# Performance work log

Measured on AMD Instinct MI355X. Metric: run time of the kernel, lower is better.

The kernel has to match this reference:

```python
import jax, jax.numpy as jnp
import numpy as np


def _bipolarize(x):
    # torchhd.hard_quantize: sign quantize to {-1, +1}
    return jnp.where(x > 0, 1.0, -1.0).astype(x.dtype)


def _transform(am, projections):
    """PQ-HDC Algorithm 1: MAP AM (C,D) -> binary AM (C,P,D) in {0,1} + weights (C,P)."""
    C, D = am.shape

    def per_class(hv):  # hv: (D,)
        bips = []
        loss = hv
        for _ in range(projections):  # P is small (2-4), sequential by construction
            bip = _bipolarize(loss)
            dot = jnp.dot(loss, bip)
            # orthogonal projection of loss onto bip: bip * dot / ||bip||^2
            loss = loss - bip * dot / jnp.sum(bip * bip)
            bips.append(bip)
        X = jnp.stack(bips)  # (P, D) bipolar
        G = X @ X.T  # (P, P)
        w = hv @ X.T @ jnp.linalg.inv(G)  # (P,)
        # normalize: length of w[:,None]*X over full (P,D) matrix
        length = jnp.linalg.norm(w[:, None] * X)
        w = jnp.sqrt(jnp.asarray(D, hv.dtype)) * w / length
        w = w ** 2
        return X, w

    Xs, ws = jax.vmap(per_class)(am)  # (C,P,D), (C,P)
    ambin = jnp.where(Xs > 0, 1.0, 0.0).astype(am.dtype)  # binarize {0,1}
    return ambin, ws


def _phs(qbin, ambin, weights):
    """Pseudo Hamming Similarity, batched. qbin:(B,D) {0,1}; ambin:(C,P,D) {0,1}."""
    D = qbin.shape[-1]
    # equal-bit count = D - sum(q XOR a) = D - sum_q - sum_a + 2*q.a
    dots = jnp.einsum('bd,cpd->bcp', qbin, ambin)  # (B,C,P)
    qsum = jnp.sum(qbin, axis=-1)                  # (B,)
    asum = jnp.sum(ambin, axis=-1)                 # (C,P)
    ham = D - qsum[:, None, None] - asum[None, :, :] + 2.0 * dots
    return jnp.sum(weights[None, :, :] * ham, axis=-1)  # (B,C)


def setup_inputs() -> dict:
    key = jax.random.key(0)
    k1, k2 = jax.random.split(key)
    B, C, D = 4096, 128, 10000
    query = jax.random.normal(k1, (B, D), dtype=jnp.float32)
    am = jax.random.normal(k2, (C, D), dtype=jnp.float32)
    return {"query": query, "am": am, "projections": 3}


def reference(query, am, projections):
    ambin, weights = _transform(am, projections)
    qbin = jnp.where(_bipolarize(query) > 0, 1.0, 0.0).astype(query.dtype)
    return _phs(qbin, ambin, weights)  # (B, C) logits
```

## Files before the change

kernel.cpp:

```cpp
#include <hip/hip_runtime.h>
#include <stdint.h>

typedef unsigned long long u64;

#define D_DIM   10000
#define C_CLS   128
#define WPRP    192
#define NWORDS  160
#define NIT     40

__device__ __forceinline__ float wred64(float v) {
#pragma unroll
    for (int m = 1; m <= 32; m <<= 1) v += __shfl_xor(v, m);
    return v;
}
__device__ __forceinline__ int wred64i(int v) {
#pragma unroll
    for (int m = 1; m <= 32; m <<= 1) v += __shfl_xor(v, m);
    return v;
}

__device__ __forceinline__ size_t am_idx(int c, int wi, int p) {
    return ((size_t)c * 32 + (unsigned)wi / 6u) * 18 + (size_t)p * 6 + (unsigned)wi % 6u;
}

__global__ __launch_bounds__(256) void kA_transform(const float* __restrict__ am,
                                                    u64* __restrict__ amw,
                                                    float4* __restrict__ wtab)
{
    const int c = blockIdx.x;
    const int t = threadIdx.x;
    const int w = t >> 6;
    const int l = t & 63;

    __shared__ float redf[4];
    __shared__ int   sI[4][6];
    __shared__ float sF[4][3];

    const float* hvp = am + (size_t)c * D_DIM;

    float4 loss[10], hv[10];
#pragma unroll
    for (int k = 0; k < 10; ++k) {
        const int it = w + 4 * k;
        const int d0 = it * 256 + 4 * l;
        float4 x = make_float4(0.f, 0.f, 0.f, 0.f);
        if (d0 + 3 < D_DIM) x = *(const float4*)(hvp + d0);
        loss[k] = x; hv[k] = x;
    }

    int cnt[3]; float hX[3]; u64 sp[3];

#pragma unroll
    for (int p = 0; p < 3; ++p) {
        float sabs = 0.f;
#pragma unroll
        for (int k = 0; k < 10; ++k)
            sabs += fabsf(loss[k].x) + fabsf(loss[k].y) + fabsf(loss[k].z) + fabsf(loss[k].w);
        sabs = wred64(sabs);
        if (l == 0) redf[w] = sabs;
        __syncthreads();
        const float dot = redf[0] + redf[1] + redf[2] + redf[3];
        __syncthreads();
        const float dd = dot / (float)D_DIM;

        u64 bits = 0; int cc = 0; float hx = 0.f;
#pragma unroll
        for (int k = 0; k < 10; ++k) {
            const int it = w + 4 * k;
            const bool p0 = loss[k].x > 0.f;
            const bool p1 = loss[k].y > 0.f;
            const bool p2 = loss[k].z > 0.f;
            const bool p3 = loss[k].w > 0.f;
            const u64 b0 = __ballot(p0);
            const u64 b1 = __ballot(p1);
            const u64 b2 = __ballot(p2);
            const u64 b3 = __ballot(p3);
            if (l < 4) {
                const u64 bb = (l == 0) ? b0 : ((l == 1) ? b1 : ((l == 2) ? b2 : b3));
                amw[am_idx(c, it * 4 + l, p)] = bb;
            }
            bits |= ((u64)p0 << (4 * k)) | ((u64)p1 << (4 * k + 1))
                  | ((u64)p2 << (4 * k + 2)) | ((u64)p3 << (4 * k + 3));
            cc += (int)p0 + (int)p1 + (int)p2 + (int)p3;
            hx += (p0 ? hv[k].x : -hv[k].x) + (p1 ? hv[k].y : -hv[k].y)
                + (p2 ? hv[k].z : -hv[k].z) + (p3 ? hv[k].w : -hv[k].w);
            float4 L = loss[k];
            L.x -= p0 ? dd : -dd; L.y -= p1 ? dd : -dd;
            L.z -= p2 ? dd : -dd; L.w -= p3 ? dd : -dd;
            const int d0 = it * 256 + 4 * l;
            if (!(d0 + 3 < D_DIM)) L = make_float4(0.f, 0.f, 0.f, 0.f);
            loss[k] = L;
        }
        if (t < WPRP - NWORDS) amw[am_idx(c, NWORDS + t, p)] = 0ull;
        sp[p] = bits; cnt[p] = cc; hX[p] = hx;
    }

    int vi[6] = { cnt[0], cnt[1], cnt[2],
                  static_cast<int>(__popcll(sp[0] ^ sp[1])),
                  static_cast<int>(__popcll(sp[0] ^ sp[2])),
                  static_cast<int>(__popcll(sp[1] ^ sp[2])) };
#pragma unroll
    for (int i = 0; i < 6; ++i) vi[i] = wred64i(vi[i]);
    float vf[3] = { hX[0], hX[1], hX[2] };
#pragma unroll
    for (int i = 0; i < 3; ++i) vf[i] = wred64(vf[i]);
    if (l == 0) {
#pragma unroll
        for (int i = 0; i < 6; ++i) sI[w][i] = vi[i];
#pragma unroll
        for (int i = 0; i < 3; ++i) sF[w][i] = vf[i];
    }
    __syncthreads();
    if (t == 0) {
        int a0 = 0, a1 = 0, a2 = 0, X01 = 0, X02 = 0, X12 = 0;
        float h0f = 0, h1f = 0, h2f = 0;
        for (int i = 0; i < 4; ++i) {
            a0 += sI[i][0]; a1 += sI[i][1]; a2 += sI[i][2];
            X01 += sI[i][3]; X02 += sI[i][4]; X12 += sI[i][5];
            h0f += sF[i][0]; h1f += sF[i][1]; h2f += sF[i][2];
        }
        const double Dv = (double)D_DIM;
        const double h0 = h0f, h1 = h1f, h2 = h2f;
        const double g01 = Dv - 2.0 * X01, g02 = Dv - 2.0 * X02, g12 = Dv - 2.0 * X12;
        const double A00 = Dv * Dv - g12 * g12;
        const double A01 = g02 * g12 - g01 * Dv;
        const double A02 = g01 * g12 - g02 * Dv;
        const double A11 = Dv * Dv - g02 * g02;
        const double A12 = g02 * g01 - Dv * g12;
        const double A22 = Dv * Dv - g01 * g01;
        const double det = Dv * A00 + g01 * A01 + g02 * A02;
        const double w0 = (A00 * h0 + A01 * h1 + A02 * h2) / det;
        const double w1 = (A01 * h0 + A11 * h1 + A12 * h2) / det;
        const double w2 = (A02 * h0 + A12 * h1 + A22 * h2) / det;
        const double s = w0 * w0 + w1 * w1 + w2 * w2;
        const double f0 = w0 * w0 / s, f1 = w1 * w1 / s, f2 = w2 * w2 / s;
        const double cb = -(f0 * a0 + f1 * a1 + f2 * a2);
        wtab[c] = make_float4((float)f0, (float)f1, (float)f2, (float)cb);
    }
}

__global__ __launch_bounds__(256, 4) void kB_phs(const float* __restrict__ query,
                                                 const u64* __restrict__ amw,
                                                 const float4* __restrict__ wtab,
                                                 float* __restrict__ out)
{
    __shared__ u64 qlds[4 * WPRP];
    __shared__ float4 wsh[C_CLS];
    const int t = threadIdx.x;
    const int w = t >> 6;
    const int l = t & 63;
    const int r0 = blockIdx.x * 4;

    if (t < C_CLS) wsh[t] = wtab[t];

    {
        const float* qp = query + (size_t)(r0 + w) * D_DIM;
        u64* qrow = qlds + w * WPRP;
        for (int it = 0; it < NIT; ++it) {
            const int d0 = it * 256 + 4 * l;
            float4 x = make_float4(0.f, 0.f, 0.f, 0.f);
            if (d0 + 3 < D_DIM) x = *(const float4*)(qp + d0);
            const u64 b0 = __ballot(x.x > 0.f);
            const u64 b1 = __ballot(x.y > 0.f);
            const u64 b2 = __ballot(x.z > 0.f);
            const u64 b3 = __ballot(x.w > 0.f);
            if (l < 4) qrow[it * 4 + l] = (l == 0) ? b0 : ((l == 1) ? b1 : ((l == 2) ? b2 : b3));
        }
        if (l < 32) qrow[NWORDS + l] = 0ull;
    }
    __syncthreads();

    const int wl = l & 31;
    const int rh = l >> 5;
    const int rA = 2 * rh, rB = 2 * rh + 1;

    const u64* qa = qlds + rA * WPRP + wl * 6;
    const u64* qb = qlds + rB * WPRP + wl * 6;
    const u64 qa0 = qa[0], qa1 = qa[1], qa2 = qa[2], qa3 = qa[3], qa4 = qa[4], qa5 = qa[5];
    const u64 qb0 = qb[0], qb1 = qb[1], qb2 = qb[2], qb3 = qb[3], qb4 = qb[4], qb5 = qb[5];

    float sA = (float)(__popcll(qa0) + __popcll(qa1) + __popcll(qa2) +
                       __popcll(qa3) + __popcll(qa4) + __popcll(qa5));
    float sB = (float)(__popcll(qb0) + __popcll(qb1) + __popcll(qb2) +
                       __popcll(qb3) + __popcll(qb4) + __popcll(qb5));
#pragma unroll
    for (int m = 1; m <= 16; m <<= 1) { sA += __shfl_xor(sA, m); sB += __shfl_xor(sB, m); }
    const float baseA = (float)D_DIM - sA;
    const float baseB = (float)D_DIM - sB;

    float* orowA = out + (size_t)(r0 + rA) * C_CLS;
    float* orowB = out + (size_t)(r0 + rB) * C_CLS;

    const int c0 = 32 * w;
#pragma unroll 2
    for (int i = 0; i < 32; ++i) {
        const int c = c0 + i;
        const u64* ap = amw + ((size_t)c * 32 + wl) * 18;
        const ulonglong2 v0 = *(const ulonglong2*)(ap + 0);
        const ulonglong2 v1 = *(const ulonglong2*)(ap + 2);
        const ulonglong2 v2 = *(const ulonglong2*)(ap + 4);
        const ulonglong2 v3 = *(const ulonglong2*)(ap + 6);
        const ulonglong2 v4 = *(const ulonglong2*)(ap + 8);
        const ulonglong2 v5 = *(const ulonglong2*)(ap + 10);
        const ulonglong2 v6 = *(const ulonglong2*)(ap + 12);
        const ulonglong2 v7 = *(const ulonglong2*)(ap + 14);
        const ulonglong2 v8 = *(const ulonglong2*)(ap + 16);

        const int pA0 = (int)(__popcll(qa0 & v0.x) + __popcll(qa1 & v0.y) + __popcll(qa2 & v1.x)
                      + __popcll(qa3 & v1.y) + __popcll(qa4 & v2.x) + __popcll(qa5 & v2.y));
        const int pA1 = (int)(__popcll(qa0 & v3.x) + __popcll(qa1 & v3.y) + __popcll(qa2 & v4.x)
                      + __popcll(qa3 & v4.y) + __popcll(qa4 & v5.x) + __popcll(qa5 & v5.y));
        const int pA2 = (int)(__popcll(qa0 & v6.x) + __popcll(qa1 & v6.y) + __popcll(qa2 & v7.x)
                      + __popcll(qa3 & v7.y) + __popcll(qa4 & v8.x) + __popcll(qa5 & v8.y));
        const int pB0 = (int)(__popcll(qb0 & v0.x) + __popcll(qb1 & v0.y) + __popcll(qb2 & v1.x)
                      + __popcll(qb3 & v1.y) + __popcll(qb4 & v2.x) + __popcll(qb5 & v2.y));
        const int pB1 = (int)(__popcll(qb0 & v3.x) + __popcll(qb1 & v3.y) + __popcll(qb2 & v4.x)
                      + __popcll(qb3 & v4.y) + __popcll(qb4 & v5.x) + __popcll(qb5 & v5.y));
        const int pB2 = (int)(__popcll(qb0 & v6.x) + __popcll(qb1 & v6.y) + __popcll(qb2 & v7.x)
                      + __popcll(qb3 & v7.y) + __popcll(qb4 & v8.x) + __popcll(qb5 & v8.y));

        const float4 wv = wsh[c];
        float partA = wv.x * (float)pA0 + wv.y * (float)pA1 + wv.z * (float)pA2;
        float partB = wv.x * (float)pB0 + wv.y * (float)pB1 + wv.z * (float)pB2;
#pragma unroll
        for (int m = 1; m <= 16; m <<= 1) {
            partA += __shfl_xor(partA, m);
            partB += __shfl_xor(partB, m);
        }
        if (wl == 0) {
            orowA[c] = baseA + wv.w + 2.f * partA;
            orowB[c] = baseB + wv.w + 2.f * partB;
        }
    }
}

extern "C" void kernel_launch(void* const* d_in, const int* in_sizes, int n_in,
                              void* d_out, int out_size, void* d_ws, size_t ws_size,
                              hipStream_t stream)
{
    const float* query = (const float*)d_in[0];
    const float* am    = (const float*)d_in[1];
    float* out = (float*)d_out;

    float4* wtab = (float4*)d_ws;
    u64* amw = (u64*)((char*)d_ws + 2048);

    const int B = in_sizes[0] / D_DIM;

    hipLaunchKernelGGL(kA_transform, dim3(C_CLS), dim3(256), 0, stream, am, amw, wtab);
    hipLaunchKernelGGL(kB_phs, dim3(B / 4), dim3(256), 0, stream, query, amw, wtab, out);
}
```

Measured before the change: 99.67 us.

## Replace per-class shuffle reductions with LDS transpose-reduce over class groups

```diff
diff --git a/kernel.cpp b/kernel.cpp
--- a/kernel.cpp
+++ b/kernel.cpp
@@ -8,6 +8,7 @@
 #define WPRP    192
 #define NWORDS  160
 #define NIT     40
+#define GRP     8
 
 __device__ __forceinline__ float wred64(float v) {
 #pragma unroll
@@ -147,6 +148,7 @@
 {
     __shared__ u64 qlds[4 * WPRP];
     __shared__ float4 wsh[C_CLS];
+    __shared__ float part[4][4][GRP][33];
     const int t = threadIdx.x;
     const int w = t >> 6;
     const int l = t & 63;
@@ -180,58 +182,72 @@
     const u64 qa0 = qa[0], qa1 = qa[1], qa2 = qa[2], qa3 = qa[3], qa4 = qa[4], qa5 = qa[5];
     const u64 qb0 = qb[0], qb1 = qb[1], qb2 = qb[2], qb3 = qb[3], qb4 = qb[4], qb5 = qb[5];
 
-    float sA = (float)(__popcll(qa0) + __popcll(qa1) + __popcll(qa2) +
-                       __popcll(qa3) + __popcll(qa4) + __popcll(qa5));
-    float sB = (float)(__popcll(qb0) + __popcll(qb1) + __popcll(qb2) +
-                       __popcll(qb3) + __popcll(qb4) + __popcll(qb5));
-#pragma unroll
-    for (int m = 1; m <= 16; m <<= 1) { sA += __shfl_xor(sA, m); sB += __shfl_xor(sB, m); }
-    const float baseA = (float)D_DIM - sA;
-    const float baseB = (float)D_DIM - sB;
-
-    float* orowA = out + (size_t)(r0 + rA) * C_CLS;
-    float* orowB = out + (size_t)(r0 + rB) * C_CLS;
+    const int qsA = (int)(__popcll(qa0) + __popcll(qa1) + __popcll(qa2) +
+                          __popcll(qa3) + __popcll(qa4) + __popcll(qa5));
+    const int qsB = (int)(__popcll(qb0) + __popcll(qb1) + __popcll(qb2) +
+                          __popcll(qb3) + __popcll(qb4) + __popcll(qb5));
+    const float offA = 312.5f - (float)qsA;
+    const float offB = 312.5f - (float)qsB;
+
+    const int o = l >> 1;
+    const int row_loc = o >> 3;
+    const int cc = o & 7;
+    const int h = l & 1;
 
     const int c0 = 32 * w;
-#pragma unroll 2
-    for (int i = 0; i < 32; ++i) {
-        const int c = c0 + i;
-        const u64* ap = amw + ((size_t)c * 32 + wl) * 18;
-        const ulonglong2 v0 = *(const ulonglong2*)(ap + 0);
-        const ulonglong2 v1 = *(const ulonglong2*)(ap + 2);
-        const ulonglong2 v2 = *(const ulonglong2*)(ap + 4);
-        const ulonglong2 v3 = *(const ulonglong2*)(ap + 6);
-        const ulonglong2 v4 = *(const ulonglong2*)(ap + 8);
-        const ulonglong2 v5 = *(const ulonglong2*)(ap + 10);
-        const ulonglong2 v6 = *(const ulonglong2*)(ap + 12);
-        const ulonglong2 v7 = *(const ulonglong2*)(ap + 14);
-        const ulonglong2 v8 = *(const ulonglong2*)(ap + 16);
-
-        const int pA0 = (int)(__popcll(qa0 & v0.x) + __popcll(qa1 & v0.y) + __popcll(qa2 & v1.x)
-                      + __popcll(qa3 & v1.y) + __popcll(qa4 & v2.x) + __popcll(qa5 & v2.y));
-        const int pA1 = (int)(__popcll(qa0 & v3.x) + __popcll(qa1 & v3.y) + __popcll(qa2 & v4.x)
-                      + __popcll(qa3 & v4.y) + __popcll(qa4 & v5.x) + __popcll(qa5 & v5.y));
-        const int pA2 = (int)(__popcll(qa0 & v6.x) + __popcll(qa1 & v6.y) + __popcll(qa2 & v7.x)
-                      + __popcll(qa3 & v7.y) + __popcll(qa4 & v8.x) + __popcll(qa5 & v8.y));
-        const int pB0 = (int)(__popcll(qb0 & v0.x) + __popcll(qb1 & v0.y) + __popcll(qb2 & v1.x)
-                      + __popcll(qb3 & v1.y) + __popcll(qb4 & v2.x) + __popcll(qb5 & v2.y));
-        const int pB1 = (int)(__popcll(qb0 & v3.x) + __popcll(qb1 & v3.y) + __popcll(qb2 & v4.x)
-                      + __popcll(qb3 & v4.y) + __popcll(qb4 & v5.x) + __popcll(qb5 & v5.y));
-        const int pB2 = (int)(__popcll(qb0 & v6.x) + __popcll(qb1 & v6.y) + __popcll(qb2 & v7.x)
-                      + __popcll(qb3 & v7.y) + __popcll(qb4 & v8.x) + __popcll(qb5 & v8.y));
-
-        const float4 wv = wsh[c];
-        float partA = wv.x * (float)pA0 + wv.y * (float)pA1 + wv.z * (float)pA2;
-        float partB = wv.x * (float)pB0 + wv.y * (float)pB1 + wv.z * (float)pB2;
-#pragma unroll
-        for (int m = 1; m <= 16; m <<= 1) {
-            partA += __shfl_xor(partA, m);
-            partB += __shfl_xor(partB, m);
-        }
-        if (wl == 0) {
-            orowA[c] = baseA + wv.w + 2.f * partA;
-            orowB[c] = baseB + wv.w + 2.f * partB;
-        }
+    float (*pw)[GRP][33] = part[w];
+
+    for (int g = 0; g < 4; ++g) {
+        float accA[GRP], accB[GRP];
+#pragma unroll
+        for (int i = 0; i < GRP; ++i) {
+            const int c = c0 + g * GRP + i;
+            const u64* ap = amw + ((size_t)c * 32 + wl) * 18;
+            const ulonglong2 v0 = *(const ulonglong2*)(ap + 0);
+            const ulonglong2 v1 = *(const ulonglong2*)(ap + 2);
+            const ulonglong2 v2 = *(const ulonglong2*)(ap + 4);
+            const ulonglong2 v3 = *(const ulonglong2*)(ap + 6);
+            const ulonglong2 v4 = *(const ulonglong2*)(ap + 8);
+            const ulonglong2 v5 = *(const ulonglong2*)(ap + 10);
+            const ulonglong2 v6 = *(const ulonglong2*)(ap + 12);
+            const ulonglong2 v7 = *(const ulonglong2*)(ap + 14);
+            const ulonglong2 v8 = *(const ulonglong2*)(ap + 16);
+
+            const int pA0 = (int)(__popcll(qa0 & v0.x) + __popcll(qa1 & v0.y) + __popcll(qa2 & v1.x)
+                          + __popcll(qa3 & v1.y) + __popcll(qa4 & v2.x) + __popcll(qa5 & v2.y));
+            const int pA1 = (int)(__popcll(qa0 & v3.x) + __popcll(qa1 & v3.y) + __popcll(qa2 & v4.x)
+                          + __popcll(qa3 & v4.y) + __popcll(qa4 & v5.x) + __popcll(qa5 & v5.y));
+            const int pA2 = (int)(__popcll(qa0 & v6.x) + __popcll(qa1 & v6.y) + __popcll(qa2 & v7.x)
+                          + __popcll(qa3 & v7.y) + __popcll(qa4 & v8.x) + __popcll(qa5 & v8.y));
+            const int pB0 = (int)(__popcll(qb0 & v0.x) + __popcll(qb1 & v0.y) + __popcll(qb2 & v1.x)
+                          + __popcll(qb3 & v1.y) + __popcll(qb4 & v2.x) + __popcll(qb5 & v2.y));
+            const int pB1 = (int)(__popcll(qb0 & v3.x) + __popcll(qb1 & v3.y) + __popcll(qb2 & v4.x)
+                          + __popcll(qb3 & v4.y) + __popcll(qb4 & v5.x) + __popcll(qb5 & v5.y));
+            const int pB2 = (int)(__popcll(qb0 & v6.x) + __popcll(qb1 & v6.y) + __popcll(qb2 & v7.x)
+                          + __popcll(qb3 & v7.y) + __popcll(qb4 & v8.x) + __popcll(qb5 & v8.y));
+
+            const float4 wv = wsh[c];
+            const float cw = wv.w * 0.03125f;
+            accA[i] = fmaf(2.f, wv.x * (float)pA0 + wv.y * (float)pA1 + wv.z * (float)pA2,
+                           offA + cw);
+            accB[i] = fmaf(2.f, wv.x * (float)pB0 + wv.y * (float)pB1 + wv.z * (float)pB2,
+                           offB + cw);
+        }
+
+#pragma unroll
+        for (int i = 0; i < GRP; ++i) {
+            pw[rA][i][wl] = accA[i];
+            pw[rB][i][wl] = accB[i];
+        }
+        __syncthreads();
+
+        float s = 0.f;
+#pragma unroll
+        for (int j = 0; j < 16; ++j) s += pw[row_loc][cc][h * 16 + j];
+        s += __shfl_xor(s, 1);
+        if (h == 0)
+            out[(size_t)(r0 + row_loc) * C_CLS + (c0 + g * GRP + cc)] = s;
+        __syncthreads();
     }
 }
 
```

After: 96.82 us. 1.03x faster.
